# Kernel optimization log

Measured on AMD Instinct MI355X. Metric: run time of the kernel, lower is better.

## Reference

```python
import jax, jax.numpy as jnp
import numpy as np

B, T1, T2, V, D, H = 1024, 256, 256, 32004, 50, 64


def _lstm_scan(x, h0, c0, Wih, Whh, b):
    """PyTorch-gate-order LSTM over time. x: [B,T,D]; returns hs, cs: [B,T,H]."""
    def step(carry, xt):
        h, c = carry
        g = xt @ Wih.T + h @ Whh.T + b  # [B, 4H], gate order i,f,g,o
        i, f, gg, o = jnp.split(g, 4, axis=-1)
        c = jax.nn.sigmoid(f) * c + jax.nn.sigmoid(i) * jnp.tanh(gg)
        h = jax.nn.sigmoid(o) * jnp.tanh(c)
        return (h, c), (h, c)
    _, (hs, cs) = jax.lax.scan(step, (h0, c0), jnp.swapaxes(x, 0, 1))
    return jnp.swapaxes(hs, 0, 1), jnp.swapaxes(cs, 0, 1)


def setup_inputs() -> dict:
    key = jax.random.key(0)
    ks = jax.random.split(key, 20)
    s = 1.0 / np.sqrt(H).astype(np.float32)
    inp = {
        "sentence1": jax.random.randint(ks[0], (B, T1), 0, V),
        "sentence2": jax.random.randint(ks[1], (B, T2), 0, V),
        "s1_len": jax.random.randint(ks[2], (B, 1, H), 0, T1),
        "s2_len": jax.random.randint(ks[3], (B, 1, H), 0, T2),
        "s1_s": jax.random.randint(ks[4], (B,), 0, 2),
        "s2_s": jax.random.randint(ks[5], (B,), 0, 2),
        "emb": jax.random.normal(ks[6], (V, D), jnp.float32),
        "Wih1": jax.random.uniform(ks[7], (4 * H, D), jnp.float32, -s, s),
        "Whh1": jax.random.uniform(ks[8], (4 * H, H), jnp.float32, -s, s),
        "bih1": jax.random.uniform(ks[9], (4 * H,), jnp.float32, -s, s),
        "bhh1": jax.random.uniform(ks[10], (4 * H,), jnp.float32, -s, s),
        "Wih2": jax.random.uniform(ks[11], (4 * H, D), jnp.float32, -s, s),
        "Whh2": jax.random.uniform(ks[12], (4 * H, H), jnp.float32, -s, s),
        "bih2": jax.random.uniform(ks[13], (4 * H,), jnp.float32, -s, s),
        "bhh2": jax.random.uniform(ks[14], (4 * H,), jnp.float32, -s, s),
        "Wl1": jax.random.uniform(ks[15], (128, H), jnp.float32, -s, s),
        "bl1": jax.random.uniform(ks[16], (128,), jnp.float32, -s, s),
        "Wl2": jax.random.uniform(ks[17], (4, 128), jnp.float32, -0.1, 0.1),
        "bl2": jax.random.uniform(ks[18], (4,), jnp.float32, -0.1, 0.1),
    }
    return inp


def reference(sentence1, sentence2, s1_len, s2_len, s1_s, s2_s, emb,
              Wih1, Whh1, bih1, bhh1, Wih2, Whh2, bih2, bhh2, Wl1, bl1, Wl2, bl2):
    embed1 = emb[sentence1]  # [B,T1,D]
    embed2 = emb[sentence2]  # [B,T2,D]
    h0 = jnp.zeros((B, H), embed1.dtype)
    c0 = jnp.zeros((B, H), embed1.dtype)
    # manual LSTMCell loop in original == scanned LSTM, keep all h,c per step
    h, c = _lstm_scan(embed1, h0, c0, Wih1, Whh1, bih1 + bhh1)  # [B,T1,H]
    gather_h = jnp.take_along_axis(h, s1_len, axis=1)[:, 0, :]  # [B,H]
    gather_c = jnp.take_along_axis(c, s1_len, axis=1)[:, 0, :]
    out, _ = _lstm_scan(embed2, gather_h, gather_c, Wih2, Whh2, bih2 + bhh2)
    out = jnp.take_along_axis(out, s2_len, axis=1)[:, 0, :]  # [B,H]
    out = jnp.tanh(out @ Wl1.T + bl1)  # dropout is identity at inference
    out = out @ Wl2.T + bl2  # [B,4]
    return out
```

## Files before the change

kernel.cpp:

```cpp
#include <hip/hip_runtime.h>

#define Bsz 1024
#define Tt  256
#define Vv  32004
#define Dd  50
#define Hh  64
#define MB  128

typedef __bf16 b16x8 __attribute__((ext_vector_type(8)));
typedef float  f32x4 __attribute__((ext_vector_type(4)));

__device__ __forceinline__ void barrier_novm() {
    asm volatile("s_waitcnt lgkmcnt(0)\n\ts_barrier" ::: "memory");
}
__device__ __forceinline__ float fexp2(float x) {
    float r;
    asm("v_exp_f32 %0, %1" : "=v"(r) : "v"(x));
    return r;
}
__device__ __forceinline__ float frcp(float x) {
    float r;
    asm("v_rcp_f32 %0, %1" : "=v"(r) : "v"(x));
    return r;
}
__device__ __forceinline__ float fsig(float x) {
    return frcp(1.0f + fexp2(x * -1.442695041f));
}
__device__ __forceinline__ float ftanh(float x) {
    return 2.0f * frcp(1.0f + fexp2(x * -2.885390082f)) - 1.0f;
}

__device__ __forceinline__ void cvt_hilo(const float* x, b16x8& hi, b16x8& lo) {
#pragma unroll
    for (int e = 0; e < 8; ++e) {
        const __bf16 h = (__bf16)x[e];
        hi[e] = h;
        lo[e] = (__bf16)(x[e] - (float)h);
    }
}

__launch_bounds__(256)
__global__ void build_tables(const float* __restrict__ emb,
                             const float* __restrict__ Wih1,
                             const float* __restrict__ bih1,
                             const float* __restrict__ bhh1,
                             const float* __restrict__ Wih2,
                             const float* __restrict__ bih2,
                             const float* __restrict__ bhh2,
                             float* __restrict__ tab1,
                             float* __restrict__ tab2) {
    const int tid  = threadIdx.x;
    const int w    = tid >> 6;
    const int lane = tid & 63;
    const int q    = lane >> 4;
    const int mn   = lane & 15;
    const int v0   = blockIdx.x * MB;

    const float* Wih = blockIdx.y ? Wih2 : Wih1;
    const float* bih = blockIdx.y ? bih2 : bih1;
    const float* bhh = blockIdx.y ? bhh2 : bhh1;
    float*       tab = blockIdx.y ? tab2 : tab1;

    __shared__ __align__(16) float wlds[256 * Dd];
    __shared__ __align__(16) float elds[MB * Dd];

    for (int d4 = tid; d4 < 256 * Dd / 4; d4 += 256)
        *(float4*)&wlds[4 * d4] = *(const float4*)(Wih + 4 * d4);
    {
        const int ebase = v0 * Dd;
        const int elim  = Vv * Dd - ebase;
        const int mx    = Vv * Dd - 1;
        for (int d4 = tid; d4 < MB * Dd / 4; d4 += 256) {
            const int d = 4 * d4;
            float4 v;
            if (d + 4 <= elim) {
                v = *(const float4*)(emb + ebase + d);
            } else {
                v.x = emb[min(ebase + d,     mx)];
                v.y = emb[min(ebase + d + 1, mx)];
                v.z = emb[min(ebase + d + 2, mx)];
                v.w = emb[min(ebase + d + 3, mx)];
            }
            *(float4*)&elds[d] = v;
        }
    }
    __syncthreads();

    b16x8 bh[4][2], bl[4][2];
    f32x4 bias4;
#pragma unroll
    for (int k = 0; k < 4; ++k) {
        const int g = 64 * k + 16 * w + mn;
        const int base = g * Dd;
        float x[8];
#pragma unroll
        for (int j = 0; j < 8; ++j) x[j] = wlds[base + 8 * q + j];
        cvt_hilo(x, bh[k][0], bl[k][0]);
#pragma unroll
        for (int j = 0; j < 8; ++j) {
            const int col = 32 + 8 * q + j;
            x[j] = (col < Dd) ? wlds[base + col] : 0.0f;
        }
        cvt_hilo(x, bh[k][1], bl[k][1]);
        bias4[k] = bih[g] + bhh[g];
    }

#pragma unroll 1
    for (int m = 0; m < MB / 16; ++m) {
        const int base = (16 * m + mn) * Dd;
        b16x8 ah[2], al[2];
        float x[8];
#pragma unroll
        for (int j = 0; j < 8; ++j) x[j] = elds[base + 8 * q + j];
        cvt_hilo(x, ah[0], al[0]);
#pragma unroll
        for (int j = 0; j < 8; ++j) {
            const int col = 32 + 8 * q + j;
            x[j] = (col < Dd) ? elds[base + col] : 0.0f;
        }
        cvt_hilo(x, ah[1], al[1]);

        f32x4 acc[4];
#pragma unroll
        for (int k = 0; k < 4; ++k) {
            f32x4 a = {0.0f, 0.0f, 0.0f, 0.0f};
#pragma unroll
            for (int kh = 0; kh < 2; ++kh) {
                a = __builtin_amdgcn_mfma_f32_16x16x32_bf16(ah[kh], bh[k][kh], a, 0, 0, 0);
                a = __builtin_amdgcn_mfma_f32_16x16x32_bf16(ah[kh], bl[k][kh], a, 0, 0, 0);
                a = __builtin_amdgcn_mfma_f32_16x16x32_bf16(al[kh], bh[k][kh], a, 0, 0, 0);
            }
            acc[k] = a;
        }
#pragma unroll
        for (int r = 0; r < 4; ++r) {
            const int vr = v0 + 16 * m + 4 * q + r;
            if (vr < Vv) {
                f32x4 o;
                o[0] = acc[0][r] + bias4[0];
                o[1] = acc[1][r] + bias4[1];
                o[2] = acc[2][r] + bias4[2];
                o[3] = acc[3][r] + bias4[3];
                *(f32x4*)(tab + (size_t)vr * 256 + (16 * w + mn) * 4) = o;
            }
        }
    }
}

__launch_bounds__(256, 1)
__global__ void lstm_main(const int*   __restrict__ s1,
                          const int*   __restrict__ s2,
                          const int*   __restrict__ len1,
                          const int*   __restrict__ len2,
                          const float* __restrict__ tab1,
                          const float* __restrict__ tab2,
                          const float* __restrict__ Whh1,
                          const float* __restrict__ Whh2,
                          const float* __restrict__ Wl1,
                          const float* __restrict__ bl1,
                          const float* __restrict__ Wl2,
                          const float* __restrict__ bl2,
                          float* __restrict__ out) {
    const int tid  = threadIdx.x;
    const int w    = tid >> 6;
    const int lane = tid & 63;
    const int q    = lane >> 4;
    const int mn   = lane & 15;
    const int row  = mn & 3;
    const bool sb0 = (mn >> 2) & 1;
    const bool sb1 = (mn >> 3) & 1;
    const int u_own = 16 * w + 4 * q + (mn >> 2);
    const int b0   = blockIdx.x * 4;

    __shared__ __align__(16) __bf16 hsh[2][4][96];
    __shared__ __align__(16) int toklds[4][Tt + 8];
    __shared__ float h2s[4][64];
    __shared__ float ys[4][128];

    float c = 0.0f, selh = 0.0f, selc = 0.0f;
    const f32x4 zero4 = {0.0f, 0.0f, 0.0f, 0.0f};

    for (int phase = 0; phase < 2; ++phase) {
        const float* tab  = phase ? tab2 : tab1;
        const float* Whh  = phase ? Whh2 : Whh1;
        const int*   sent = phase ? s2 : s1;
        const int*   lenp = phase ? len2 : len1;

        for (int i = tid; i < 4 * Tt; i += 256)
            toklds[i >> 8][i & 255] = sent[(size_t)(b0 + (i >> 8)) * Tt + (i & 255)];

        b16x8 af[8];
#pragma unroll
        for (int k = 0; k < 4; ++k) {
            const int gate = 64 * k + 16 * w + mn;
#pragma unroll
            for (int kh = 0; kh < 2; ++kh) {
                const float* ar = Whh + (size_t)gate * Hh + kh * 32 + q * 8;
                const float4 f0 = *(const float4*)ar;
                const float4 f1 = *(const float4*)(ar + 4);
                b16x8 a;
                a[0] = (__bf16)f0.x; a[1] = (__bf16)f0.y;
                a[2] = (__bf16)f0.z; a[3] = (__bf16)f0.w;
                a[4] = (__bf16)f1.x; a[5] = (__bf16)f1.y;
                a[6] = (__bf16)f1.z; a[7] = (__bf16)f1.w;
                af[2 * k + kh] = a;
            }
        }

        const int mi = lenp[(size_t)(b0 + row) * Hh + u_own];

        const float h0f = phase ? selh : 0.0f;
        c = phase ? selc : 0.0f;
        hsh[0][row][u_own] = (__bf16)h0f;
        selh = 0.0f; selc = 0.0f;
        __syncthreads();

        const float* tu = tab + 4 * u_own;

        int4 tk0 = *(const int4*)&toklds[row][0];
        int4 tkA = *(const int4*)&toklds[row][4];
        int4 tkB = *(const int4*)&toklds[row][8];

        f32x4 S0, S1, S2, S3, S4, S5, S6, S7;
        S0 = *(const f32x4*)(tu + (size_t)tk0.x * 256);
        S1 = *(const f32x4*)(tu + (size_t)tk0.y * 256);
        S2 = *(const f32x4*)(tu + (size_t)tk0.z * 256);
        S3 = *(const f32x4*)(tu + (size_t)tk0.w * 256);

        auto pick = [&](const f32x4& a) -> float {
            const float e01 = sb0 ? a[1] : a[0];
            const float e23 = sb0 ? a[3] : a[2];
            return sb1 ? e23 : e01;
        };

        auto step = [&](int i, f32x4& Su, f32x4& Sf, int tok, int tb) {
            Sf = *(const f32x4*)(tu + (size_t)tok * 256);

            const int rb = i & 1, wb = rb ^ 1;
            const b16x8 bf0 = *(const b16x8*)&hsh[rb][row][q * 8];
            const b16x8 bf1 = *(const b16x8*)&hsh[rb][row][32 + q * 8];

            f32x4 aG = __builtin_amdgcn_mfma_f32_16x16x32_bf16(af[4], bf0, zero4, 0, 0, 0);
            aG = __builtin_amdgcn_mfma_f32_16x16x32_bf16(af[5], bf1, aG, 0, 0, 0);
            f32x4 aI = __builtin_amdgcn_mfma_f32_16x16x32_bf16(af[0], bf0, zero4, 0, 0, 0);
            aI = __builtin_amdgcn_mfma_f32_16x16x32_bf16(af[1], bf1, aI, 0, 0, 0);
            f32x4 aF = __builtin_amdgcn_mfma_f32_16x16x32_bf16(af[2], bf0, zero4, 0, 0, 0);
            aF = __builtin_amdgcn_mfma_f32_16x16x32_bf16(af[3], bf1, aF, 0, 0, 0);
            f32x4 aO = __builtin_amdgcn_mfma_f32_16x16x32_bf16(af[6], bf0, zero4, 0, 0, 0);
            aO = __builtin_amdgcn_mfma_f32_16x16x32_bf16(af[7], bf1, aO, 0, 0, 0);

            const float gG = pick(aG) + Su[2];
            const float gI = pick(aI) + Su[0];
            const float gF = pick(aF) + Su[1];
            const float gO = pick(aO) + Su[3];

            const float gv = ftanh(gG);
            const float iv = fsig(gI);
            const float fv = fsig(gF);
            const float ov = fsig(gO);
            c = fv * c + iv * gv;
            const float hv = ov * ftanh(c);
            hsh[wb][row][u_own] = (__bf16)hv;
            if (tb + i == mi) { selh = hv; selc = c; }
            barrier_novm();
        };

        for (int tb = 0; tb < Tt; tb += 8) {
            step(0, S0, S4, tkA.x, tb);
            step(1, S1, S5, tkA.y, tb);
            const int nb1 = min(tb + 12, Tt - 4);
            const int4 tA2 = *(const int4*)&toklds[row][nb1];
            step(2, S2, S6, tkA.z, tb);
            const int nb2 = min(tb + 16, Tt - 4);
            const int4 tB2 = *(const int4*)&toklds[row][nb2];
            step(3, S3, S7, tkA.w, tb);
            step(4, S4, S0, tkB.x, tb);
            step(5, S5, S1, tkB.y, tb);
            step(6, S6, S2, tkB.z, tb);
            step(7, S7, S3, tkB.w, tb);
            tkA = tA2; tkB = tB2;
        }
    }

    h2s[row][u_own] = selh;
    __syncthreads();
#pragma unroll
    for (int p = 0; p < 2; ++p) {
        const int idx = tid + 256 * p;
        const int rr = idx >> 7, n = idx & 127;
        float a = bl1[n];
        const float* wl = Wl1 + n * 64;
#pragma unroll 8
        for (int k = 0; k < 64; ++k) a += h2s[rr][k] * wl[k];
        ys[rr][n] = ftanh(a);
    }
    __syncthreads();
    if (tid < 16) {
        const int rr = tid >> 2, o = tid & 3;
        float a = bl2[o];
        const float* wl = Wl2 + o * 128;
#pragma unroll 8
        for (int k = 0; k < 128; ++k) a += ys[rr][k] * wl[k];
        out[(size_t)(b0 + rr) * 4 + o] = a;
    }
}

extern "C" void kernel_launch(void* const* d_in, const int* in_sizes, int n_in,
                              void* d_out, int out_size, void* d_ws, size_t ws_size,
                              hipStream_t stream) {
    const int*   s1   = (const int*)d_in[0];
    const int*   s2   = (const int*)d_in[1];
    const int*   l1   = (const int*)d_in[2];
    const int*   l2   = (const int*)d_in[3];
    const float* emb  = (const float*)d_in[6];
    const float* Wih1 = (const float*)d_in[7];
    const float* Whh1 = (const float*)d_in[8];
    const float* bih1 = (const float*)d_in[9];
    const float* bhh1 = (const float*)d_in[10];
    const float* Wih2 = (const float*)d_in[11];
    const float* Whh2 = (const float*)d_in[12];
    const float* bih2 = (const float*)d_in[13];
    const float* bhh2 = (const float*)d_in[14];
    const float* Wl1  = (const float*)d_in[15];
    const float* bl1  = (const float*)d_in[16];
    const float* Wl2  = (const float*)d_in[17];
    const float* bl2  = (const float*)d_in[18];
    float* out = (float*)d_out;

    float* tab1 = (float*)d_ws;
    float* tab2 = tab1 + (size_t)Vv * 256;

    dim3 grid((Vv + MB - 1) / MB, 2);
    build_tables<<<grid, 256, 0, stream>>>(emb, Wih1, bih1, bhh1,
                                           Wih2, bih2, bhh2, tab1, tab2);
    lstm_main<<<Bsz / 4, 256, 0, stream>>>(s1, s2, l1, l2, tab1, tab2,
                                           Whh1, Whh2, Wl1, bl1, Wl2, bl2, out);
}
```

Before: 259.7 us.

## Give each wave its own batch row to drop per-step block barriers

Each wavefront now owns one whole batch row and computes all 256 gates for it with 32 MFMAs per step. Previously the four waves split the gates of four rows and had to exchange h through double-buffered LDS with a block barrier every timestep. The recurrent state now stays private to each wave in a single LDS row buffer, so the per-step s_barrier is removed. The cost is four times as many MFMAs per wave per step, most of their output columns unused, plus more registers held for weight fragments and accumulators.

```diff
diff --git a/kernel.cpp b/kernel.cpp
--- a/kernel.cpp
+++ b/kernel.cpp
@@ -10,9 +10,6 @@
 typedef __bf16 b16x8 __attribute__((ext_vector_type(8)));
 typedef float  f32x4 __attribute__((ext_vector_type(4)));
 
-__device__ __forceinline__ void barrier_novm() {
-    asm volatile("s_waitcnt lgkmcnt(0)\n\ts_barrier" ::: "memory");
-}
 __device__ __forceinline__ float fexp2(float x) {
     float r;
     asm("v_exp_f32 %0, %1" : "=v"(r) : "v"(x));
@@ -166,13 +163,14 @@
     const int lane = tid & 63;
     const int q    = lane >> 4;
     const int mn   = lane & 15;
-    const int row  = mn & 3;
+    const bool sr0 = mn & 1;
+    const bool sr1 = (mn >> 1) & 1;
     const bool sb0 = (mn >> 2) & 1;
     const bool sb1 = (mn >> 3) & 1;
-    const int u_own = 16 * w + 4 * q + (mn >> 2);
-    const int b0   = blockIdx.x * 4;
-
-    __shared__ __align__(16) __bf16 hsh[2][4][96];
+    const int u_own = 16 * (mn & 3) + 4 * q + (mn >> 2);
+    const int rowg  = blockIdx.x * 4 + w;
+
+    __shared__ __align__(16) __bf16 hrow[4][80];
     __shared__ __align__(16) int toklds[4][Tt + 8];
     __shared__ float h2s[4][64];
     __shared__ float ys[4][128];
@@ -186,40 +184,43 @@
         const int*   sent = phase ? s2 : s1;
         const int*   lenp = phase ? len2 : len1;
 
+        __syncthreads();
         for (int i = tid; i < 4 * Tt; i += 256)
-            toklds[i >> 8][i & 255] = sent[(size_t)(b0 + (i >> 8)) * Tt + (i & 255)];
-
-        b16x8 af[8];
-#pragma unroll
-        for (int k = 0; k < 4; ++k) {
-            const int gate = 64 * k + 16 * w + mn;
-#pragma unroll
-            for (int kh = 0; kh < 2; ++kh) {
-                const float* ar = Whh + (size_t)gate * Hh + kh * 32 + q * 8;
-                const float4 f0 = *(const float4*)ar;
-                const float4 f1 = *(const float4*)(ar + 4);
-                b16x8 a;
-                a[0] = (__bf16)f0.x; a[1] = (__bf16)f0.y;
-                a[2] = (__bf16)f0.z; a[3] = (__bf16)f0.w;
-                a[4] = (__bf16)f1.x; a[5] = (__bf16)f1.y;
-                a[6] = (__bf16)f1.z; a[7] = (__bf16)f1.w;
-                af[2 * k + kh] = a;
-            }
-        }
-
-        const int mi = lenp[(size_t)(b0 + row) * Hh + u_own];
+            toklds[i >> 8][i & 255] = sent[(size_t)(blockIdx.x * 4 + (i >> 8)) * Tt + (i & 255)];
+
+        b16x8 af[4][4][2];
+#pragma unroll
+        for (int g = 0; g < 4; ++g)
+#pragma unroll
+            for (int s = 0; s < 4; ++s) {
+                const int gate = 64 * g + 16 * s + mn;
+#pragma unroll
+                for (int kh = 0; kh < 2; ++kh) {
+                    const float* ar = Whh + (size_t)gate * Hh + kh * 32 + q * 8;
+                    const float4 f0 = *(const float4*)ar;
+                    const float4 f1 = *(const float4*)(ar + 4);
+                    b16x8 a;
+                    a[0] = (__bf16)f0.x; a[1] = (__bf16)f0.y;
+                    a[2] = (__bf16)f0.z; a[3] = (__bf16)f0.w;
+                    a[4] = (__bf16)f1.x; a[5] = (__bf16)f1.y;
+                    a[6] = (__bf16)f1.z; a[7] = (__bf16)f1.w;
+                    af[g][s][kh] = a;
+                }
+            }
+
+        const int mi = lenp[(size_t)rowg * Hh + u_own];
 
         const float h0f = phase ? selh : 0.0f;
         c = phase ? selc : 0.0f;
-        hsh[0][row][u_own] = (__bf16)h0f;
+        hrow[w][u_own] = (__bf16)h0f;
         selh = 0.0f; selc = 0.0f;
         __syncthreads();
 
         const float* tu = tab + 4 * u_own;
 
-        int4 tk0 = *(const int4*)&toklds[row][0];
-        int4 tkA = *(const int4*)&toklds[row][4];
-        int4 tkB = *(const int4*)&toklds[row][8];
+        int4 tk0 = *(const int4*)&toklds[w][0];
+        int4 tkA = *(const int4*)&toklds[w][4];
+        int4 tkB = *(const int4*)&toklds[w][8];
 
         f32x4 S0, S1, S2, S3, S4, S5, S6, S7;
         S0 = *(const f32x4*)(tu + (size_t)tk0.x * 256);
@@ -227,32 +228,49 @@
         S2 = *(const f32x4*)(tu + (size_t)tk0.z * 256);
         S3 = *(const f32x4*)(tu + (size_t)tk0.w * 256);
 
-        auto pick = [&](const f32x4& a) -> float {
-            const float e01 = sb0 ? a[1] : a[0];
-            const float e23 = sb0 ? a[3] : a[2];
-            return sb1 ? e23 : e01;
+        auto pick = [&](const f32x4& a0, const f32x4& a1,
+                        const f32x4& a2, const f32x4& a3) -> float {
+            const float e0 = sb1 ? (sb0 ? a0[3] : a0[2]) : (sb0 ? a0[1] : a0[0]);
+            const float e1 = sb1 ? (sb0 ? a1[3] : a1[2]) : (sb0 ? a1[1] : a1[0]);
+            const float e2 = sb1 ? (sb0 ? a2[3] : a2[2]) : (sb0 ? a2[1] : a2[0]);
+            const float e3 = sb1 ? (sb0 ? a3[3] : a3[2]) : (sb0 ? a3[1] : a3[0]);
+            const float t01 = sr0 ? e1 : e0;
+            const float t23 = sr0 ? e3 : e2;
+            return sr1 ? t23 : t01;
         };
 
         auto step = [&](int i, f32x4& Su, f32x4& Sf, int tok, int tb) {
             Sf = *(const f32x4*)(tu + (size_t)tok * 256);
 
-            const int rb = i & 1, wb = rb ^ 1;
-            const b16x8 bf0 = *(const b16x8*)&hsh[rb][row][q * 8];
-            const b16x8 bf1 = *(const b16x8*)&hsh[rb][row][32 + q * 8];
-
-            f32x4 aG = __builtin_amdgcn_mfma_f32_16x16x32_bf16(af[4], bf0, zero4, 0, 0, 0);
-            aG = __builtin_amdgcn_mfma_f32_16x16x32_bf16(af[5], bf1, aG, 0, 0, 0);
-            f32x4 aI = __builtin_amdgcn_mfma_f32_16x16x32_bf16(af[0], bf0, zero4, 0, 0, 0);
-            aI = __builtin_amdgcn_mfma_f32_16x16x32_bf16(af[1], bf1, aI, 0, 0, 0);
-            f32x4 aF = __builtin_amdgcn_mfma_f32_16x16x32_bf16(af[2], bf0, zero4, 0, 0, 0);
-            aF = __builtin_amdgcn_mfma_f32_16x16x32_bf16(af[3], bf1, aF, 0, 0, 0);
-            f32x4 aO = __builtin_amdgcn_mfma_f32_16x16x32_bf16(af[6], bf0, zero4, 0, 0, 0);
-            aO = __builtin_amdgcn_mfma_f32_16x16x32_bf16(af[7], bf1, aO, 0, 0, 0);
-
-            const float gG = pick(aG) + Su[2];
-            const float gI = pick(aI) + Su[0];
-            const float gF = pick(aF) + Su[1];
-            const float gO = pick(aO) + Su[3];
+            const b16x8 bf0 = *(const b16x8*)&hrow[w][q * 8];
+            const b16x8 bf1 = *(const b16x8*)&hrow[w][32 + q * 8];
+
+            f32x4 aG[4], aI[4], aF[4], aO[4];
+#pragma unroll
+            for (int s = 0; s < 4; ++s) {
+                aG[s] = __builtin_amdgcn_mfma_f32_16x16x32_bf16(af[2][s][0], bf0, zero4, 0, 0, 0);
+                aG[s] = __builtin_amdgcn_mfma_f32_16x16x32_bf16(af[2][s][1], bf1, aG[s], 0, 0, 0);
+            }
+#pragma unroll
+            for (int s = 0; s < 4; ++s) {
+                aI[s] = __builtin_amdgcn_mfma_f32_16x16x32_bf16(af[0][s][0], bf0, zero4, 0, 0, 0);
+                aI[s] = __builtin_amdgcn_mfma_f32_16x16x32_bf16(af[0][s][1], bf1, aI[s], 0, 0, 0);
+            }
+#pragma unroll
+            for (int s = 0; s < 4; ++s) {
+                aF[s] = __builtin_amdgcn_mfma_f32_16x16x32_bf16(af[1][s][0], bf0, zero4, 0, 0, 0);
+                aF[s] = __builtin_amdgcn_mfma_f32_16x16x32_bf16(af[1][s][1], bf1, aF[s], 0, 0, 0);
+            }
+#pragma unroll
+            for (int s = 0; s < 4; ++s) {
+                aO[s] = __builtin_amdgcn_mfma_f32_16x16x32_bf16(af[3][s][0], bf0, zero4, 0, 0, 0);
+                aO[s] = __builtin_amdgcn_mfma_f32_16x16x32_bf16(af[3][s][1], bf1, aO[s], 0, 0, 0);
+            }
+
+            const float gG = pick(aG[0], aG[1], aG[2], aG[3]) + Su[2];
+            const float gI = pick(aI[0], aI[1], aI[2], aI[3]) + Su[0];
+            const float gF = pick(aF[0], aF[1], aF[2], aF[3]) + Su[1];
+            const float gO = pick(aO[0], aO[1], aO[2], aO[3]) + Su[3];
 
             const float gv = ftanh(gG);
             const float iv = fsig(gI);
@@ -260,19 +278,18 @@
             const float ov = fsig(gO);
             c = fv * c + iv * gv;
             const float hv = ov * ftanh(c);
-            hsh[wb][row][u_own] = (__bf16)hv;
+            hrow[w][u_own] = (__bf16)hv;
             if (tb + i == mi) { selh = hv; selc = c; }
-            barrier_novm();
         };
 
         for (int tb = 0; tb < Tt; tb += 8) {
             step(0, S0, S4, tkA.x, tb);
             step(1, S1, S5, tkA.y, tb);
             const int nb1 = min(tb + 12, Tt - 4);
-            const int4 tA2 = *(const int4*)&toklds[row][nb1];
+            const int4 tA2 = *(const int4*)&toklds[w][nb1];
             step(2, S2, S6, tkA.z, tb);
             const int nb2 = min(tb + 16, Tt - 4);
-            const int4 tB2 = *(const int4*)&toklds[row][nb2];
+            const int4 tB2 = *(const int4*)&toklds[w][nb2];
             step(3, S3, S7, tkA.w, tb);
             step(4, S4, S0, tkB.x, tb);
             step(5, S5, S1, tkB.y, tb);
@@ -282,7 +299,7 @@
         }
     }
 
-    h2s[row][u_own] = selh;
+    h2s[w][u_own] = selh;
     __syncthreads();
 #pragma unroll
     for (int p = 0; p < 2; ++p) {
@@ -301,7 +318,7 @@
         const float* wl = Wl2 + o * 128;
 #pragma unroll 8
         for (int k = 0; k < 128; ++k) a += ys[rr][k] * wl[k];
-        out[(size_t)(b0 + rr) * 4 + o] = a;
+        out[(size_t)(blockIdx.x * 4 + rr) * 4 + o] = a;
     }
 }
 
```

Result: slower. 402.1 us (+54.8%).
